# Kernel tuning notes

Hardware: AMD Instinct MI355X
Metric: run time of the kernel (lower is better)

The kernel has to match this reference:

```python
import jax, jax.numpy as jnp
import numpy as np
from jax import lax

B, CIN, H, W = 64, 3, 224, 224
FEAT = 64          # conv output channels after pooling
OUT = 1024         # output_dim


def _conv2d(x, w, b, stride):
    # x: NCHW, w: OIHW, padding=1, stride=stride
    y = lax.conv_general_dilated(
        x, w, window_strides=(stride, stride), padding=((1, 1), (1, 1)),
        dimension_numbers=("NCHW", "OIHW", "NCHW"))
    return y + b[None, :, None, None]


def setup_inputs() -> dict:
    key = jax.random.key(0)
    ks = jax.random.split(key, 12)
    s = 0.05
    return {
        "x": jax.random.normal(ks[0], (B, CIN, H, W), dtype=jnp.float32),
        "w1": jax.random.normal(ks[1], (32, CIN, 3, 3), dtype=jnp.float32) * s,
        "b1": jax.random.normal(ks[2], (32,), dtype=jnp.float32) * s,
        "w2": jax.random.normal(ks[3], (64, 32, 3, 3), dtype=jnp.float32) * s,
        "b2": jax.random.normal(ks[4], (64,), dtype=jnp.float32) * s,
        "wm": jax.random.normal(ks[5], (OUT, FEAT), dtype=jnp.float32) * s,
        "bm": jax.random.normal(ks[6], (OUT,), dtype=jnp.float32) * s,
        "wc": jax.random.normal(ks[7], (OUT, FEAT * FEAT), dtype=jnp.float32) * s,
        "bc": jax.random.normal(ks[8], (OUT,), dtype=jnp.float32) * s,
        "w3": jax.random.normal(ks[9], (OUT, FEAT ** 3), dtype=jnp.float32) * s,
        "b3": jax.random.normal(ks[10], (OUT,), dtype=jnp.float32) * s,
    }


def reference(x, w1, b1, w2, b2, wm, bm, wc, bc, w3, b3):
    # conv trunk: conv3x3 s2 -> relu -> conv3x3 s2 -> relu -> global avg pool
    h = jax.nn.relu(_conv2d(x, w1, b1, 2))
    h = jax.nn.relu(_conv2d(h, w2, b2, 2))
    feat = jnp.mean(h, axis=(2, 3))                    # (B, 64)

    mean_feat = feat @ wm.T + bm                       # (B, OUT)

    fc = feat - jnp.mean(feat, axis=1, keepdims=True)  # centered (B, 64)

    # 2nd-order: outer product flattened -> linear
    cov = (fc[:, :, None] * fc[:, None, :]).reshape(B, FEAT * FEAT)
    cov_feat = cov @ wc.T + bc

    # 3rd-order: rank-1 third-order outer product flattened -> linear
    outer3 = (fc[:, :, None, None] * fc[:, None, :, None] * fc[:, None, None, :])
    third_feat = outer3.reshape(B, FEAT ** 3) @ w3.T + b3

    return mean_feat + cov_feat + third_feat
```

## Files before the change

### kernel.cpp

```cpp
#include <hip/hip_runtime.h>
#include <hip/hip_bf16.h>

#define BB   64
#define CIN  3
#define HH   224
#define WW   224
#define C1   32
#define H1   112
#define W1   112
#define C2   64
#define H2   56
#define W2   56
#define FEATN 64
#define OUTN 1024
#define K3TOT (FEATN*FEATN*FEATN)

typedef __bf16 bf16x8 __attribute__((ext_vector_type(8)));
typedef float  f32x4  __attribute__((ext_vector_type(4)));
typedef unsigned int u32;

__device__ __forceinline__ void gload_lds16(const void* g, void* l) {
  __builtin_amdgcn_global_load_lds((const __attribute__((address_space(1))) u32*)g,
                                   (__attribute__((address_space(3))) u32*)l, 16, 0, 0);
}
__device__ __forceinline__ void gload_lds16_nt(const void* g, void* l) {
  __builtin_amdgcn_global_load_lds((const __attribute__((address_space(1))) u32*)g,
                                   (__attribute__((address_space(3))) u32*)l, 16, 0, 2);
}

__global__ __launch_bounds__(256) void prep_kernel(__bf16* __restrict__ h1T,
        const float* __restrict__ w2, __bf16* __restrict__ wf) {
    int gid = blockIdx.x * 256 + threadIdx.x;
    if (gid < 64 * 452) {
      int b = gid / 452, s = gid - b * 452;
      int row, col;
      if      (s < 114) { row = 0;        col = s; }
      else if (s < 228) { row = 113;      col = s - 114; }
      else if (s < 340) { row = s - 227;  col = 0; }
      else              { row = s - 339;  col = 113; }
      __bf16* p = h1T + (((size_t)b * 114 + row) * 114 + col) * 32;
      bf16x8 z = {};
      #pragma unroll
      for (int k = 0; k < 4; ++k) *(bf16x8*)(p + k * 8) = z;
    } else if (gid < 64 * 452 + 18432) {
      int t = gid - 64 * 452;
      int e    = t & 7;
      int lane = (t >> 3) & 63;
      int q    = (t >> 9) % 9;
      int j    = t / 4608;
      int oc = j * 16 + (lane & 15);
      int c  = (lane >> 4) * 8 + e;
      wf[t] = (__bf16)w2[(oc * C1 + c) * 9 + q];
    }
}

__global__ __launch_bounds__(256) void conv1_kernel(const float* __restrict__ x,
        const float* __restrict__ w1, const float* __restrict__ b1,
        __bf16* __restrict__ h1T) {
    int pos = blockIdx.x * 256 + threadIdx.x;
    int b   = pos / (H1 * 56);
    int rem = pos - b * (H1 * 56);
    int oy  = rem / 56;
    int g   = rem - oy * 56;
    int iy0 = oy * 2 - 1;

    float win[CIN][3][5];
    #pragma unroll
    for (int c = 0; c < CIN; ++c)
      #pragma unroll
      for (int dy = 0; dy < 3; ++dy) {
        int iy = iy0 + dy;
        bool rv = (iy >= 0) & (iy < HH);
        const float* row = x + ((size_t)(b * CIN + c) * HH + (rv ? iy : 0)) * WW;
        float lf = (rv && g > 0) ? row[4 * g - 1] : 0.f;
        float4 f4 = rv ? *(const float4*)(row + 4 * g) : (float4){0.f, 0.f, 0.f, 0.f};
        win[c][dy][0] = lf;
        win[c][dy][1] = f4.x; win[c][dy][2] = f4.y;
        win[c][dy][3] = f4.z; win[c][dy][4] = f4.w;
      }

    float acc[2][C1];
    #pragma unroll
    for (int u = 0; u < 2; ++u)
      #pragma unroll
      for (int oc = 0; oc < C1; ++oc) acc[u][oc] = b1[oc];

    #pragma unroll
    for (int c = 0; c < CIN; ++c)
      #pragma unroll
      for (int dy = 0; dy < 3; ++dy)
        #pragma unroll
        for (int dx = 0; dx < 3; ++dx) {
          float w0 = win[c][dy][dx];
          float w1v = win[c][dy][dx + 2];
          const float* wq = w1 + c * 9 + dy * 3 + dx;
          #pragma unroll
          for (int oc = 0; oc < C1; ++oc) {
            float wv = wq[oc * 27];
            acc[0][oc] = fmaf(wv, w0, acc[0][oc]);
            acc[1][oc] = fmaf(wv, w1v, acc[1][oc]);
          }
        }

    __bf16* dst = h1T + (((size_t)b * 114 + oy + 1) * 114 + (2 * g) + 1) * 32;
    #pragma unroll
    for (int u = 0; u < 2; ++u) {
      bf16x8 outv[4];
      #pragma unroll
      for (int k = 0; k < 32; ++k)
        outv[k >> 3][k & 7] = (__bf16)fmaxf(acc[u][k], 0.f);
      #pragma unroll
      for (int k = 0; k < 4; ++k) *(bf16x8*)(dst + u * 32 + k * 8) = outv[k];
    }
}

__global__ __launch_bounds__(256) void conv2_kernel(const __bf16* __restrict__ h1T,
        const __bf16* __restrict__ wf, const float* __restrict__ b2,
        float* __restrict__ featp) {
    __shared__ __align__(16) char tile[2304 * 16];
    __shared__ float pool_red[4][64];
    int t = threadIdx.x;
    int bid = blockIdx.x;
    int b  = bid / 28;
    int yt = bid - b * 28;
    int y0 = yt * 2;
    int w = t >> 6, lane = t & 63, l15 = lane & 15, l4 = lane >> 4;

    const char* src_base = (const char*)(h1T + ((size_t)b * 114 + 2 * y0) * 114 * 32);
    #pragma unroll
    for (int i = 0; i < 9; ++i) {
      int g = (w * 9 + i) * 64 + lane;
      int site = g >> 2; site = site < 569 ? site : 569;
      int qp = g & 3;
      int r5 = site / 114;
      int col = site - r5 * 114;
      int ql = (qp - col) & 3;
      gload_lds16(src_base + (size_t)site * 64 + ql * 16, tile + (size_t)g * 16);
    }
    __syncthreads();

    int sbase[2], urot[2];
    #pragma unroll
    for (int p = 0; p < 2; ++p) {
      int mt = 2 * w + p;
      int yl = mt >> 2;
      int xl = ((mt & 3) << 4) + l15;
      int xe = xl < 55 ? xl : 55;
      sbase[p] = ((yl * 2) * 114 + 2 * xe) * 64;
      urot[p]  = (l4 + 2 * xe) & 3;
    }

    f32x4 acc[2][4];
    #pragma unroll
    for (int p = 0; p < 2; ++p)
      #pragma unroll
      for (int j = 0; j < 4; ++j) acc[p][j] = (f32x4){0.f, 0.f, 0.f, 0.f};

    #pragma unroll
    for (int q = 0; q < 9; ++q) {
      int dy = q / 3, dx = q % 3;
      bf16x8 bw[4];
      #pragma unroll
      for (int j = 0; j < 4; ++j)
        bw[j] = *(const bf16x8*)(wf + ((j * 9 + q) * 64 + lane) * 8);
      bf16x8 af[2];
      #pragma unroll
      for (int p = 0; p < 2; ++p) {
        int addr = sbase[p] + (dy * 114 + dx) * 64 + (((urot[p] + dx) & 3) << 4);
        af[p] = *(const bf16x8*)(tile + addr);
      }
      #pragma unroll
      for (int p = 0; p < 2; ++p)
        #pragma unroll
        for (int j = 0; j < 4; ++j)
          acc[p][j] = __builtin_amdgcn_mfma_f32_16x16x32_bf16(af[p], bw[j], acc[p][j], 0, 0, 0);
    }

    float bias[4];
    #pragma unroll
    for (int j = 0; j < 4; ++j) bias[j] = b2[j * 16 + l15];
    float ps[4] = {0.f, 0.f, 0.f, 0.f};
    #pragma unroll
    for (int p = 0; p < 2; ++p) {
      int mt = 2 * w + p;
      bool valid = ((mt & 3) != 3) || (l4 < 2);
      #pragma unroll
      for (int j = 0; j < 4; ++j) {
        float sj = 0.f;
        #pragma unroll
        for (int r = 0; r < 4; ++r)
          sj += fmaxf(acc[p][j][r] + bias[j], 0.f);
        ps[j] += valid ? sj : 0.f;
      }
    }
    #pragma unroll
    for (int j = 0; j < 4; ++j) {
      ps[j] += __shfl_xor(ps[j], 16);
      ps[j] += __shfl_xor(ps[j], 32);
    }
    if (l4 == 0) {
      #pragma unroll
      for (int j = 0; j < 4; ++j) pool_red[w][j * 16 + l15] = ps[j];
    }
    __syncthreads();
    if (t < 64) {
      float s = pool_red[0][t] + pool_red[1][t] + pool_red[2][t] + pool_red[3][t];
      featp[((size_t)yt * 64 + b) * 64 + t] = s;
    }
}

__global__ __launch_bounds__(64) void center2_kernel(const float* __restrict__ featp,
        float* __restrict__ featN, float* __restrict__ fc) {
    int b = blockIdx.x;
    int c = threadIdx.x;
    float s = 0.f;
    #pragma unroll 7
    for (int yt = 0; yt < 28; ++yt)
      s += featp[((size_t)yt * 64 + b) * 64 + c];
    s *= (1.f / (H2 * W2));
    float tot = s;
    #pragma unroll
    for (int off = 32; off; off >>= 1) tot += __shfl_xor(tot, off);
    featN[b * 64 + c] = s;
    fc[b * 64 + c]    = s - tot * (1.f / 64.f);
}

#define T3_NBLK 32
#define KSLICES 128
#define CHUNK_IJ 2
#define NCHUNK 16
#define T3_GRID (T3_NBLK * KSLICES)

struct T3Shared {
    float stage[2][32][CHUNK_IJ*64];
    float fcJ[32][65];
    float fcI[64];
};

__device__ __forceinline__ void t3_issue(const char* w3b, float (*buf)[CHUNK_IJ*64],
        int wave, int ocolbase, size_t kb, int lane) {
    int hi = lane >> 5;
    int lo = (lane & 31) * 16;
    #pragma unroll
    for (int i = 0; i < 8; ++i) {
      int colb = wave*16 + 2*i;
      int col  = colb + hi;
      int srcoff = lo ^ ((col & 7) << 4);
      const char* src = w3b + (((size_t)(ocolbase + col)) << 20) + kb + srcoff;
      gload_lds16_nt(src, &buf[colb][0]);
    }
}

__device__ __forceinline__ void t3_compute(const float (*buf)[CHUNK_IJ*64],
        const float (*fcJ)[65], const float* fcI,
        int c, int wave, int lane, const float4 aA[4][2], const float4 aB[4][2],
        f32x4 acc[4]) {
    int l15 = lane & 15, l4 = lane >> 4;
    int col = wave*16 + l15;
    int swz = (col & 7) << 4;
    int x0 = (l4*32) ^ swz;
    int x1 = (l4*32 + 16) ^ swz;
    const char* p = (const char*)&buf[col][0];
    #pragma unroll
    for (int e = 0; e < CHUNK_IJ; ++e) {
      int jl = c*CHUNK_IJ + e;
      float smul[4];
      #pragma unroll
      for (int m = 0; m < 4; ++m) {
        int bb = m*16 + l15;
        smul[m] = fcI[bb] * fcJ[jl][bb];
      }
      #pragma unroll
      for (int s = 0; s < 2; ++s) {
        int K = e*256 + s*128;
        float4 b0 = *(const float4*)(p + K + x0);
        float4 b1 = *(const float4*)(p + K + x1);
        bf16x8 bfrag;
        bfrag[0] = (__bf16)b0.x; bfrag[1] = (__bf16)b0.y;
        bfrag[2] = (__bf16)b0.z; bfrag[3] = (__bf16)b0.w;
        bfrag[4] = (__bf16)b1.x; bfrag[5] = (__bf16)b1.y;
        bfrag[6] = (__bf16)b1.z; bfrag[7] = (__bf16)b1.w;
        #pragma unroll
        for (int m = 0; m < 4; ++m) {
          float sc = smul[m];
          bf16x8 afrag;
          afrag[0] = (__bf16)(aA[m][s].x * sc); afrag[1] = (__bf16)(aA[m][s].y * sc);
          afrag[2] = (__bf16)(aA[m][s].z * sc); afrag[3] = (__bf16)(aA[m][s].w * sc);
          afrag[4] = (__bf16)(aB[m][s].x * sc); afrag[5] = (__bf16)(aB[m][s].y * sc);
          afrag[6] = (__bf16)(aB[m][s].z * sc); afrag[7] = (__bf16)(aB[m][s].w * sc);
          acc[m] = __builtin_amdgcn_mfma_f32_16x16x32_bf16(afrag, bfrag, acc[m], 0, 0, 0);
        }
      }
    }
}

#define T3_WAIT(N) do { asm volatile("s_waitcnt vmcnt(" #N ")" ::: "memory"); \
                        __builtin_amdgcn_sched_barrier(0); } while (0)

__global__ __launch_bounds__(128) void third_kernel(const float* __restrict__ fc,
        const float* __restrict__ w3, float* __restrict__ part) {
    __shared__ T3Shared sh;
    int t = threadIdx.x;
    int nblk   = blockIdx.x >> 7;
    int kslice = blockIdx.x & 127;
    int i0     = kslice >> 1;
    int jbase  = (kslice & 1) * 32;

    for (int idx = t; idx < 32*64; idx += 128) {
      int b = idx >> 5, jl = idx & 31;
      sh.fcJ[jl][b] = fc[b*64 + jbase + jl];
    }
    if (t < 64) sh.fcI[t] = fc[t*64 + i0];
    __syncthreads();

    int wave = t >> 6;
    int lane = t & 63;
    int l15  = lane & 15;
    int l4   = lane >> 4;
    int ocolbase = nblk * 32;

    float4 aA[4][2], aB[4][2];
    #pragma unroll
    for (int m = 0; m < 4; ++m)
      #pragma unroll
      for (int s = 0; s < 2; ++s) {
        const float* pa = fc + (m*16 + l15)*64 + (s*4 + l4)*8;
        aA[m][s] = *(const float4*)pa;
        aB[m][s] = *(const float4*)(pa + 4);
      }

    f32x4 acc[4];
    #pragma unroll
    for (int m = 0; m < 4; ++m) acc[m] = (f32x4){0.f, 0.f, 0.f, 0.f};

    const char* w3b = (const char*)w3;
    size_t kb0 = (size_t)kslice * 8192;
    #define KB(c) (kb0 + (size_t)(c) * (CHUNK_IJ*64*4))

    t3_issue(w3b, sh.stage[0], wave, ocolbase, KB(0), lane);
    #pragma unroll 1
    for (int c = 0; c < NCHUNK - 2; c += 2) {
      t3_issue(w3b, sh.stage[1], wave, ocolbase, KB(c+1), lane);
      T3_WAIT(8);
      t3_compute(sh.stage[0], sh.fcJ, sh.fcI, c, wave, lane, aA, aB, acc);
      t3_issue(w3b, sh.stage[0], wave, ocolbase, KB(c+2), lane);
      T3_WAIT(8);
      t3_compute(sh.stage[1], sh.fcJ, sh.fcI, c+1, wave, lane, aA, aB, acc);
    }
    t3_issue(w3b, sh.stage[1], wave, ocolbase, KB(NCHUNK-1), lane);
    T3_WAIT(8);
    t3_compute(sh.stage[0], sh.fcJ, sh.fcI, NCHUNK-2, wave, lane, aA, aB, acc);
    T3_WAIT(0);
    t3_compute(sh.stage[1], sh.fcJ, sh.fcI, NCHUNK-1, wave, lane, aA, aB, acc);

    float* pt = part + (size_t)kslice * 64 * OUTN;
    int ocol = ocolbase + wave*16 + l15;
    #pragma unroll
    for (int m = 0; m < 4; ++m) {
      float4 v = {acc[m][0], acc[m][1], acc[m][2], acc[m][3]};
      *(float4*)&pt[(size_t)ocol * 64 + m * 16 + l4 * 4] = v;
    }
}

__global__ __launch_bounds__(256) void finale_kernel(const float* __restrict__ feat,
        const float* __restrict__ fc,
        const float* __restrict__ wm, const float* __restrict__ bm,
        const float* __restrict__ wc, const float* __restrict__ bcv,
        const float* __restrict__ b3, const float* __restrict__ part,
        float* __restrict__ out) {
    __shared__ float featT[FEATN * FEATN];
    __shared__ float fcT[FEATN * FEATN];
    int t = threadIdx.x;
    for (int i = t; i < FEATN * FEATN; i += 256) {
      int b = i >> 6, c = i & 63;
      featT[c*64 + b] = feat[i];
      fcT[c*64 + b]   = fc[i];
    }
    __syncthreads();

    int b = t & 63;
    int o = blockIdx.x * 4 + (t >> 6);

    float fr[64];
    #pragma unroll
    for (int c4 = 0; c4 < 16; ++c4) {
      float4 v = *(const float4*)(fc + b*64 + c4*4);
      fr[c4*4+0]=v.x; fr[c4*4+1]=v.y; fr[c4*4+2]=v.z; fr[c4*4+3]=v.w;
    }

    float acc = bm[o] + bcv[o] + b3[o];
    #pragma unroll 8
    for (int c = 0; c < FEATN; ++c)
      acc = fmaf(featT[c*64 + b], wm[o*FEATN + c], acc);

    const float* wcrow = wc + (size_t)o * (FEATN * FEATN);
    #pragma unroll 1
    for (int c1 = 0; c1 < 64; ++c1) {
      float a2 = 0.f;
      #pragma unroll
      for (int c2 = 0; c2 < 64; ++c2)
        a2 = fmaf(fr[c2], wcrow[c1*64 + c2], a2);
      acc = fmaf(fcT[c1*64 + b], a2, acc);
    }

    float s = 0.f;
    #pragma unroll 8
    for (int ks = 0; ks < KSLICES; ++ks)
      s += part[(size_t)ks * (64 * OUTN) + o * 64 + b];

    out[b * OUTN + o] = acc + s;
}

extern "C" void kernel_launch(void* const* d_in, const int* in_sizes, int n_in,
                              void* d_out, int out_size, void* d_ws, size_t ws_size,
                              hipStream_t stream) {
    const float* x   = (const float*)d_in[0];
    const float* w1  = (const float*)d_in[1];
    const float* b1  = (const float*)d_in[2];
    const float* w2  = (const float*)d_in[3];
    const float* b2  = (const float*)d_in[4];
    const float* wm  = (const float*)d_in[5];
    const float* bm  = (const float*)d_in[6];
    const float* wc  = (const float*)d_in[7];
    const float* bcv = (const float*)d_in[8];
    const float* w3  = (const float*)d_in[9];
    const float* b3  = (const float*)d_in[10];
    float* out = (float*)d_out;

    float* ws    = (float*)d_ws;
    __bf16* h1T  = (__bf16*)ws;
    float* featp = ws + 13307904;
    float* featN = ws + 13422592;
    float* fcv   = ws + 13426688;
    float* part  = ws + 13430784;
    __bf16* wfrg = (__bf16*)(ws + 21819392);

    prep_kernel   <<<185,  256, 0, stream>>>(h1T, w2, wfrg);
    conv1_kernel  <<<1568, 256, 0, stream>>>(x, w1, b1, h1T);
    conv2_kernel  <<<1792, 256, 0, stream>>>(h1T, wfrg, b2, featp);
    center2_kernel<<<64,   64,  0, stream>>>(featp, featN, fcv);
    third_kernel  <<<T3_GRID, 128, 0, stream>>>(fcv, w3, part);
    finale_kernel <<<256,  256, 0, stream>>>(featN, fcv, wm, bm, wc, bcv, b3, part, out);
}
```

Before: 358.1 us.

## Restructure third-order contraction: one block per output, fold fc factors after MFMA

The third-order kernel now assigns one block per output column. It multiplies 16-row weight chunks by fc in an MFMA, then contracts the result with fc[j] and fc[i] in registers, instead of scaling the A operand by fc_i*fc_j per (i,j). This removes the 128-slice partial-sum buffer (about 32 MB written and then read by the finale) and the k-slice reduction in the finale. The cost is a grid of only 1024 blocks with 2 waves each streaming 1 MB of weights, plus extra scalar FMA and LDS reads for the fc contraction, which may leave less memory-level parallelism.

```diff
diff --git a/kernel.cpp b/kernel.cpp
--- a/kernel.cpp
+++ b/kernel.cpp
@@ -225,148 +225,120 @@
     fc[b * 64 + c]    = s - tot * (1.f / 64.f);
 }
 
-#define T3_NBLK 32
-#define KSLICES 128
-#define CHUNK_IJ 2
-#define NCHUNK 16
-#define T3_GRID (T3_NBLK * KSLICES)
-
-struct T3Shared {
-    float stage[2][32][CHUNK_IJ*64];
-    float fcJ[32][65];
-    float fcI[64];
+#define T3_NCH 128
+
+struct T3S {
+    float stage[2][2][16][64];
+    float fcT[64][66];
+    float wred[2][64];
 };
 
-__device__ __forceinline__ void t3_issue(const char* w3b, float (*buf)[CHUNK_IJ*64],
-        int wave, int ocolbase, size_t kb, int lane) {
-    int hi = lane >> 5;
-    int lo = (lane & 31) * 16;
-    #pragma unroll
-    for (int i = 0; i < 8; ++i) {
-      int colb = wave*16 + 2*i;
-      int col  = colb + hi;
-      int srcoff = lo ^ ((col & 7) << 4);
-      const char* src = w3b + (((size_t)(ocolbase + col)) << 20) + kb + srcoff;
-      gload_lds16_nt(src, &buf[colb][0]);
-    }
-}
-
-__device__ __forceinline__ void t3_compute(const float (*buf)[CHUNK_IJ*64],
-        const float (*fcJ)[65], const float* fcI,
-        int c, int wave, int lane, const float4 aA[4][2], const float4 aB[4][2],
-        f32x4 acc[4]) {
-    int l15 = lane & 15, l4 = lane >> 4;
-    int col = wave*16 + l15;
-    int swz = (col & 7) << 4;
-    int x0 = (l4*32) ^ swz;
-    int x1 = (l4*32 + 16) ^ swz;
-    const char* p = (const char*)&buf[col][0];
-    #pragma unroll
-    for (int e = 0; e < CHUNK_IJ; ++e) {
-      int jl = c*CHUNK_IJ + e;
-      float smul[4];
-      #pragma unroll
-      for (int m = 0; m < 4; ++m) {
-        int bb = m*16 + l15;
-        smul[m] = fcI[bb] * fcJ[jl][bb];
-      }
-      #pragma unroll
-      for (int s = 0; s < 2; ++s) {
-        int K = e*256 + s*128;
-        float4 b0 = *(const float4*)(p + K + x0);
-        float4 b1 = *(const float4*)(p + K + x1);
-        bf16x8 bfrag;
-        bfrag[0] = (__bf16)b0.x; bfrag[1] = (__bf16)b0.y;
-        bfrag[2] = (__bf16)b0.z; bfrag[3] = (__bf16)b0.w;
-        bfrag[4] = (__bf16)b1.x; bfrag[5] = (__bf16)b1.y;
-        bfrag[6] = (__bf16)b1.z; bfrag[7] = (__bf16)b1.w;
-        #pragma unroll
-        for (int m = 0; m < 4; ++m) {
-          float sc = smul[m];
-          bf16x8 afrag;
-          afrag[0] = (__bf16)(aA[m][s].x * sc); afrag[1] = (__bf16)(aA[m][s].y * sc);
-          afrag[2] = (__bf16)(aA[m][s].z * sc); afrag[3] = (__bf16)(aA[m][s].w * sc);
-          afrag[4] = (__bf16)(aB[m][s].x * sc); afrag[5] = (__bf16)(aB[m][s].y * sc);
-          afrag[6] = (__bf16)(aB[m][s].z * sc); afrag[7] = (__bf16)(aB[m][s].w * sc);
-          acc[m] = __builtin_amdgcn_mfma_f32_16x16x32_bf16(afrag, bfrag, acc[m], 0, 0, 0);
+__global__ __launch_bounds__(128) void third_kernel(const float* __restrict__ fc,
+        const float* __restrict__ w3, float* __restrict__ thrd) {
+    __shared__ __align__(16) T3S sh;
+    int t = threadIdx.x;
+    int w = t >> 6, lane = t & 63, l15 = lane & 15, l4 = lane >> 4;
+    int o = blockIdx.x;
+    int swz = (l15 & 7) << 4;
+
+    for (int idx = t; idx < 4096; idx += 128)
+      sh.fcT[idx & 63][idx >> 6] = fc[idx];
+
+    const char* seg = (const char*)w3 + ((size_t)o << 20) + (size_t)w * 524288;
+
+    #pragma unroll
+    for (int ii = 0; ii < 4; ++ii) {
+      int row = ii * 4 + (lane >> 4);
+      int lo  = (lane & 15) * 16;
+      gload_lds16_nt(seg + row * 256 + (lo ^ ((row & 7) << 4)),
+                     (char*)&sh.stage[w][0][0][0] + ii * 1024);
+    }
+
+    bf16x8 bfrag[2][4];
+    #pragma unroll
+    for (int ks = 0; ks < 2; ++ks)
+      #pragma unroll
+      for (int nt = 0; nt < 4; ++nt) {
+        const float* p = fc + (nt * 16 + l15) * 64 + ks * 32 + l4 * 8;
+        float4 v0 = *(const float4*)p;
+        float4 v1 = *(const float4*)(p + 4);
+        bfrag[ks][nt][0] = (__bf16)v0.x; bfrag[ks][nt][1] = (__bf16)v0.y;
+        bfrag[ks][nt][2] = (__bf16)v0.z; bfrag[ks][nt][3] = (__bf16)v0.w;
+        bfrag[ks][nt][4] = (__bf16)v1.x; bfrag[ks][nt][5] = (__bf16)v1.y;
+        bfrag[ks][nt][6] = (__bf16)v1.z; bfrag[ks][nt][7] = (__bf16)v1.w;
+      }
+
+    __syncthreads();
+
+    float oacc[4] = {0.f, 0.f, 0.f, 0.f};
+
+    #pragma unroll 1
+    for (int c = 0; c < T3_NCH; ++c) {
+      if (c + 1 < T3_NCH) {
+        const char* s2 = seg + (size_t)(c + 1) * 4096;
+        char* db = (char*)&sh.stage[w][(c + 1) & 1][0][0];
+        #pragma unroll
+        for (int ii = 0; ii < 4; ++ii) {
+          int row = ii * 4 + (lane >> 4);
+          int lo  = (lane & 15) * 16;
+          gload_lds16_nt(s2 + row * 256 + (lo ^ ((row & 7) << 4)), db + ii * 1024);
         }
-      }
-    }
-}
-
-#define T3_WAIT(N) do { asm volatile("s_waitcnt vmcnt(" #N ")" ::: "memory"); \
-                        __builtin_amdgcn_sched_barrier(0); } while (0)
-
-__global__ __launch_bounds__(128) void third_kernel(const float* __restrict__ fc,
-        const float* __restrict__ w3, float* __restrict__ part) {
-    __shared__ T3Shared sh;
-    int t = threadIdx.x;
-    int nblk   = blockIdx.x >> 7;
-    int kslice = blockIdx.x & 127;
-    int i0     = kslice >> 1;
-    int jbase  = (kslice & 1) * 32;
-
-    for (int idx = t; idx < 32*64; idx += 128) {
-      int b = idx >> 5, jl = idx & 31;
-      sh.fcJ[jl][b] = fc[b*64 + jbase + jl];
-    }
-    if (t < 64) sh.fcI[t] = fc[t*64 + i0];
+        asm volatile("s_waitcnt vmcnt(4)" ::: "memory");
+      } else {
+        asm volatile("s_waitcnt vmcnt(0)" ::: "memory");
+      }
+      __builtin_amdgcn_sched_barrier(0);
+
+      const char* cb = (const char*)&sh.stage[w][c & 1][0][0];
+      f32x4 acc[4];
+      #pragma unroll
+      for (int nt = 0; nt < 4; ++nt) acc[nt] = (f32x4){0.f, 0.f, 0.f, 0.f};
+      #pragma unroll
+      for (int ks = 0; ks < 2; ++ks) {
+        int off0 = l15 * 256 + ((ks * 128 + l4 * 32) ^ swz);
+        float4 a0 = *(const float4*)(cb + off0);
+        float4 a1 = *(const float4*)(cb + (off0 ^ 16));
+        bf16x8 af;
+        af[0] = (__bf16)a0.x; af[1] = (__bf16)a0.y;
+        af[2] = (__bf16)a0.z; af[3] = (__bf16)a0.w;
+        af[4] = (__bf16)a1.x; af[5] = (__bf16)a1.y;
+        af[6] = (__bf16)a1.z; af[7] = (__bf16)a1.w;
+        #pragma unroll
+        for (int nt = 0; nt < 4; ++nt)
+          acc[nt] = __builtin_amdgcn_mfma_f32_16x16x32_bf16(af, bfrag[ks][nt], acc[nt], 0, 0, 0);
+      }
+      int i = w * 32 + (c >> 2);
+      #pragma unroll
+      for (int nt = 0; nt < 4; ++nt) {
+        int b = nt * 16 + l15;
+        float s = 0.f;
+        #pragma unroll
+        for (int r = 0; r < 4; ++r) {
+          int j = (c * 16 + l4 * 4 + r) & 63;
+          s = fmaf(sh.fcT[j][b], acc[nt][r], s);
+        }
+        oacc[nt] = fmaf(sh.fcT[i][b], s, oacc[nt]);
+      }
+    }
+
+    #pragma unroll
+    for (int nt = 0; nt < 4; ++nt) {
+      oacc[nt] += __shfl_xor(oacc[nt], 16);
+      oacc[nt] += __shfl_xor(oacc[nt], 32);
+    }
+    if (l4 == 0) {
+      #pragma unroll
+      for (int nt = 0; nt < 4; ++nt) sh.wred[w][nt * 16 + l15] = oacc[nt];
+    }
     __syncthreads();
-
-    int wave = t >> 6;
-    int lane = t & 63;
-    int l15  = lane & 15;
-    int l4   = lane >> 4;
-    int ocolbase = nblk * 32;
-
-    float4 aA[4][2], aB[4][2];
-    #pragma unroll
-    for (int m = 0; m < 4; ++m)
-      #pragma unroll
-      for (int s = 0; s < 2; ++s) {
-        const float* pa = fc + (m*16 + l15)*64 + (s*4 + l4)*8;
-        aA[m][s] = *(const float4*)pa;
-        aB[m][s] = *(const float4*)(pa + 4);
-      }
-
-    f32x4 acc[4];
-    #pragma unroll
-    for (int m = 0; m < 4; ++m) acc[m] = (f32x4){0.f, 0.f, 0.f, 0.f};
-
-    const char* w3b = (const char*)w3;
-    size_t kb0 = (size_t)kslice * 8192;
-    #define KB(c) (kb0 + (size_t)(c) * (CHUNK_IJ*64*4))
-
-    t3_issue(w3b, sh.stage[0], wave, ocolbase, KB(0), lane);
-    #pragma unroll 1
-    for (int c = 0; c < NCHUNK - 2; c += 2) {
-      t3_issue(w3b, sh.stage[1], wave, ocolbase, KB(c+1), lane);
-      T3_WAIT(8);
-      t3_compute(sh.stage[0], sh.fcJ, sh.fcI, c, wave, lane, aA, aB, acc);
-      t3_issue(w3b, sh.stage[0], wave, ocolbase, KB(c+2), lane);
-      T3_WAIT(8);
-      t3_compute(sh.stage[1], sh.fcJ, sh.fcI, c+1, wave, lane, aA, aB, acc);
-    }
-    t3_issue(w3b, sh.stage[1], wave, ocolbase, KB(NCHUNK-1), lane);
-    T3_WAIT(8);
-    t3_compute(sh.stage[0], sh.fcJ, sh.fcI, NCHUNK-2, wave, lane, aA, aB, acc);
-    T3_WAIT(0);
-    t3_compute(sh.stage[1], sh.fcJ, sh.fcI, NCHUNK-1, wave, lane, aA, aB, acc);
-
-    float* pt = part + (size_t)kslice * 64 * OUTN;
-    int ocol = ocolbase + wave*16 + l15;
-    #pragma unroll
-    for (int m = 0; m < 4; ++m) {
-      float4 v = {acc[m][0], acc[m][1], acc[m][2], acc[m][3]};
-      *(float4*)&pt[(size_t)ocol * 64 + m * 16 + l4 * 4] = v;
-    }
+    if (t < 64) thrd[o * 64 + t] = sh.wred[0][t] + sh.wred[1][t];
 }
 
 __global__ __launch_bounds__(256) void finale_kernel(const float* __restrict__ feat,
         const float* __restrict__ fc,
         const float* __restrict__ wm, const float* __restrict__ bm,
         const float* __restrict__ wc, const float* __restrict__ bcv,
-        const float* __restrict__ b3, const float* __restrict__ part,
+        const float* __restrict__ b3, const float* __restrict__ thrd,
         float* __restrict__ out) {
     __shared__ float featT[FEATN * FEATN];
     __shared__ float fcT[FEATN * FEATN];
@@ -403,12 +375,7 @@
       acc = fmaf(fcT[c1*64 + b], a2, acc);
     }
 
-    float s = 0.f;
-    #pragma unroll 8
-    for (int ks = 0; ks < KSLICES; ++ks)
-      s += part[(size_t)ks * (64 * OUTN) + o * 64 + b];
-
-    out[b * OUTN + o] = acc + s;
+    out[b * OUTN + o] = acc + thrd[o * 64 + b];
 }
 
 extern "C" void kernel_launch(void* const* d_in, const int* in_sizes, int n_in,
@@ -432,13 +399,13 @@
     float* featp = ws + 13307904;
     float* featN = ws + 13422592;
     float* fcv   = ws + 13426688;
-    float* part  = ws + 13430784;
-    __bf16* wfrg = (__bf16*)(ws + 21819392);
+    float* thrd  = ws + 13430784;
+    __bf16* wfrg = (__bf16*)(ws + 13496320);
 
     prep_kernel   <<<185,  256, 0, stream>>>(h1T, w2, wfrg);
     conv1_kernel  <<<1568, 256, 0, stream>>>(x, w1, b1, h1T);
     conv2_kernel  <<<1792, 256, 0, stream>>>(h1T, wfrg, b2, featp);
     center2_kernel<<<64,   64,  0, stream>>>(featp, featN, fcv);
-    third_kernel  <<<T3_GRID, 128, 0, stream>>>(fcv, w3, part);
-    finale_kernel <<<256,  256, 0, stream>>>(featN, fcv, wm, bm, wc, bcv, b3, part, out);
-}
+    third_kernel  <<<1024, 128, 0, stream>>>(fcv, w3, thrd);
+    finale_kernel <<<256,  256, 0, stream>>>(featN, fcv, wm, bm, wc, bcv, b3, thrd, out);
+}
```

Result: faster. 295.6 us, median of 2 (-17.5%).
